# Kernel tuning notes

Measured on AMD Instinct MI355X. Metric: run time of the kernel, lower is better.

The kernel has to match this reference:

```python
import jax, jax.numpy as jnp
import numpy as np

N = 40000   # nodes
E = 640000  # edges (avg degree 16)
D = 128     # in_dim
G = 64      # graphs in batch
C = 100     # n_classes
L = 3       # hidden_layers + 1 AGNN layers
EPS = 1e-12 # F.normalize eps


def setup_inputs() -> dict:
    key = jax.random.key(0)
    ks = jax.random.split(key, 6)
    h = jax.random.normal(ks[0], (N, D), jnp.float32)
    src = jax.random.randint(ks[1], (E,), 0, N, jnp.int32)
    dst = jax.random.randint(ks[2], (E,), 0, N, jnp.int32)
    graph_ids = jnp.sort(jax.random.randint(ks[3], (N,), 0, G, jnp.int32))
    betas = jnp.ones((L,), jnp.float32)  # init_beta=1.0, one learnable beta per AGNNConv
    W_cls = jax.random.normal(ks[4], (D, C), jnp.float32) / np.sqrt(D)
    b_cls = jnp.zeros((C,), jnp.float32)
    return dict(h=h, src=src, dst=dst, graph_ids=graph_ids,
                betas=betas, W_cls=W_cls, b_cls=b_cls)


def agnn_layer(h, src, dst, beta):
    # cosine-similarity attention (DGL AGNNConv)
    nh = h / (jnp.linalg.norm(h, axis=-1, keepdims=True) + EPS)  # [N, D]
    s = beta * jnp.sum(nh[src] * nh[dst], axis=-1)               # [E] edge scores
    # segment softmax over incoming edges of each dst node
    m = jax.ops.segment_max(s, dst, num_segments=N)              # [N]
    m = jnp.where(jnp.isfinite(m), m, 0.0)                       # empty segments -> 0
    a = jnp.exp(s - m[dst])                                      # [E]
    denom = jax.ops.segment_sum(a, dst, num_segments=N)          # [N]
    num = jax.ops.segment_sum(a[:, None] * h[src], dst, num_segments=N)  # [N, D]
    return num / jnp.where(denom > 0, denom, 1.0)[:, None]


def reference(h, src, dst, graph_ids, betas, W_cls, b_cls):
    # dropout is identity at inference; batch_norms are unused in the original forward
    for l in range(L):
        h = agnn_layer(h, src, dst, betas[l])
    # AvgPooling readout: per-graph mean of node features
    hg = jax.ops.segment_sum(h, graph_ids, num_segments=G)       # [G, D]
    cnt = jax.ops.segment_sum(jnp.ones((N,), h.dtype), graph_ids, num_segments=G)
    hg = hg / jnp.maximum(cnt, 1.0)[:, None]
    return hg @ W_cls + b_cls                                    # [G, C]
```

## Files before the change

### kernel.cpp

```cpp
#include <hip/hip_runtime.h>
#include <hip/hip_fp16.h>
#include <math.h>

#define N_NODES 40000
#define N_EDGES 640000
#define DIM     128
#define N_GRAPHS 64
#define N_CLS   100
#define N_LAYERS 3
#define EPSN    1e-12f


__global__ void k_zero_int(int* __restrict__ a, int n) {
    int i = blockIdx.x * blockDim.x + threadIdx.x;
    if (i < n) a[i] = 0;
}

__global__ void k_count(const int* __restrict__ dst, int* __restrict__ counts,
                        int* __restrict__ posw) {
    int e = blockIdx.x * blockDim.x + threadIdx.x;
    if (e < N_EDGES) posw[e] = atomicAdd(&counts[dst[e]], 1);
}

#define SCAN_T 1024
#define SCAN_V 40
__global__ void k_scan(const int* __restrict__ counts, int* __restrict__ offsets) {
    __shared__ int lds[SCAN_T];
    int t = threadIdx.x;
    int base = t * SCAN_V;
    int tsum = 0;
    if (base < N_NODES) {
        for (int k = 0; k < SCAN_V; ++k) tsum += counts[base + k];
    }
    lds[t] = tsum; __syncthreads();
    int x = tsum;
    for (int off = 1; off < SCAN_T; off <<= 1) {
        int y = (t >= off) ? lds[t - off] : 0;
        __syncthreads();
        x += y;
        lds[t] = x;
        __syncthreads();
    }
    int excl = x - tsum;
    if (base < N_NODES) {
        int run = excl;
        for (int k = 0; k < SCAN_V; ++k) {
            offsets[base + k] = run;
            run += counts[base + k];
        }
    }
    if (t == (N_NODES / SCAN_V)) offsets[N_NODES] = excl;
}

__global__ void k_scatter(const int* __restrict__ src, const int* __restrict__ dst,
                          const int* __restrict__ offsets, const int* __restrict__ posw,
                          int* __restrict__ csr_src) {
    int e = blockIdx.x * blockDim.x + threadIdx.x;
    if (e >= N_EDGES) return;
    csr_src[offsets[dst[e]] + posw[e]] = src[e];
}


__global__ void k_norm(const float* __restrict__ h, float* __restrict__ inv,
                       __half2* __restrict__ hh) {
    int node = (blockIdx.x * blockDim.x + threadIdx.x) >> 6;
    int lane = threadIdx.x & 63;
    if (node >= N_NODES) return;
    const float2* r2 = (const float2*)(h + (size_t)node * DIM);
    float2 v = r2[lane];
    float ss = v.x * v.x + v.y * v.y;
    #pragma unroll
    for (int o = 32; o; o >>= 1) ss += __shfl_xor(ss, o);
    if (lane == 0) inv[node] = 1.0f / (sqrtf(ss) + EPSN);
    hh[(size_t)node * 64 + lane] = __floats2half2_rn(v.x, v.y);
}

union H8 { int4 i4; __half2 h2[4]; };

__device__ __forceinline__ void cvt8(const H8& u, float* f) {
    #pragma unroll
    for (int k = 0; k < 4; ++k) {
        float2 v = __half22float2(u.h2[k]);
        f[2 * k]     = v.x;
        f[2 * k + 1] = v.y;
    }
}

template <bool LAST>
__global__ void k_fused(const int4* __restrict__ hh_in,
                        const float* __restrict__ inv_in,
                        const int* __restrict__ csr_src,
                        const int* __restrict__ offsets,
                        const float* __restrict__ betas, int layer,
                        int4* __restrict__ hh_out,
                        float* __restrict__ inv_out,
                        const int* __restrict__ gid,
                        float* __restrict__ hgsum) {
    int node = (blockIdx.x * blockDim.x + threadIdx.x) >> 6;
    int lane = threadIdx.x & 63;
    int grp = lane >> 4;
    int t   = lane & 15;

    int off = offsets[node];
    int deg = offsets[node + 1] - off;

    size_t nrow16 = (size_t)node * 16;
    H8 selfu; selfu.i4 = hh_in[nrow16 + t];
    float hd[8]; cvt8(selfu, hd);
    float bi = betas[layer] * inv_in[node];

    float dsum = 0.f;
    float ac[8];
    #pragma unroll
    for (int k = 0; k < 8; ++k) ac[k] = 0.f;

    if (deg > 0) {
        int last = deg - 1;
        int jb = 0;
        for (; jb + 8 <= deg; jb += 8) {
            int s0 = csr_src[off + jb + grp];
            int s1 = csr_src[off + jb + 4 + grp];
            H8 u0, u1;
            u0.i4 = hh_in[(size_t)s0 * 16 + t];
            u1.i4 = hh_in[(size_t)s1 * 16 + t];
            float iv0 = inv_in[s0], iv1 = inv_in[s1];
            float f0[8], f1[8];
            cvt8(u0, f0); cvt8(u1, f1);
            float p0 = 0.f, p1 = 0.f;
            #pragma unroll
            for (int k = 0; k < 8; ++k) { p0 += f0[k] * hd[k]; p1 += f1[k] * hd[k]; }
            #pragma unroll
            for (int o = 8; o; o >>= 1) {
                p0 += __shfl_xor(p0, o);
                p1 += __shfl_xor(p1, o);
            }
            float w0 = __expf(bi * iv0 * p0);
            float w1 = __expf(bi * iv1 * p1);
            dsum += w0 + w1;
            #pragma unroll
            for (int k = 0; k < 8; ++k) ac[k] += w0 * f0[k] + w1 * f1[k];
        }
        for (; jb < deg; jb += 4) {
            int j = jb + grp;
            bool valid = j <= last;
            int idx = valid ? j : last;
            int s = csr_src[off + idx];
            H8 u; u.i4 = hh_in[(size_t)s * 16 + t];
            float iv = inv_in[s];
            float f[8]; cvt8(u, f);
            float p = 0.f;
            #pragma unroll
            for (int k = 0; k < 8; ++k) p += f[k] * hd[k];
            #pragma unroll
            for (int o = 8; o; o >>= 1) p += __shfl_xor(p, o);
            float w = valid ? __expf(bi * iv * p) : 0.f;
            dsum += w;
            #pragma unroll
            for (int k = 0; k < 8; ++k) ac[k] += w * f[k];
        }

        #pragma unroll
        for (int o = 16; o < 64; o <<= 1) {
            dsum += __shfl_xor(dsum, o);
            #pragma unroll
            for (int k = 0; k < 8; ++k) ac[k] += __shfl_xor(ac[k], o);
        }
        float invd = 1.0f / dsum;
        #pragma unroll
        for (int k = 0; k < 8; ++k) ac[k] *= invd;
    }

    if (LAST) {
        __shared__ float spool[DIM];
        __shared__ int sg[4];
        int tid = threadIdx.x;
        int g = gid[node];
        if (lane == 0) sg[tid >> 6] = g;
        if (tid < DIM) spool[tid] = 0.f;
        __syncthreads();
        bool uni = (sg[0] == sg[1]) && (sg[1] == sg[2]) && (sg[2] == sg[3]);
        if (uni) {
            if (grp == 0) {
                #pragma unroll
                for (int k = 0; k < 8; ++k) atomicAdd(&spool[8 * t + k], ac[k]);
            }
            __syncthreads();
            if (tid < DIM) atomicAdd(&hgsum[(size_t)sg[0] * DIM + tid], spool[tid]);
        } else {
            if (grp == 0) {
                #pragma unroll
                for (int k = 0; k < 8; ++k)
                    atomicAdd(&hgsum[(size_t)g * DIM + 8 * t + k], ac[k]);
            }
        }
    } else {
        if (grp == 0) {
            H8 w;
            #pragma unroll
            for (int k = 0; k < 4; ++k)
                w.h2[k] = __floats2half2_rn(ac[2 * k], ac[2 * k + 1]);
            hh_out[nrow16 + t] = w.i4;
        }
        float ss = 0.f;
        #pragma unroll
        for (int k = 0; k < 8; ++k) ss += ac[k] * ac[k];
        #pragma unroll
        for (int o = 8; o; o >>= 1) ss += __shfl_xor(ss, o);
        if (lane == 0) inv_out[node] = 1.0f / (sqrtf(ss) + EPSN);
    }
}


__global__ void k_cls(const float* __restrict__ hgsum, const int* __restrict__ gid,
                      const float* __restrict__ W, const float* __restrict__ b,
                      float* __restrict__ out) {
    int g = blockIdx.x;
    int c = threadIdx.x;
    __shared__ float invc_s;
    if (c == 0) {
        int lo = 0, hi = N_NODES;
        while (lo < hi) { int mid = (lo + hi) >> 1; if (gid[mid] < g) lo = mid + 1; else hi = mid; }
        int start = lo;
        lo = 0; hi = N_NODES;
        while (lo < hi) { int mid = (lo + hi) >> 1; if (gid[mid] < g + 1) lo = mid + 1; else hi = mid; }
        invc_s = 1.0f / fmaxf((float)(lo - start), 1.0f);
    }
    __syncthreads();
    if (c >= N_CLS) return;
    float acc = 0.f;
    #pragma unroll 8
    for (int d = 0; d < DIM; ++d) acc += hgsum[g * DIM + d] * W[d * N_CLS + c];
    out[g * N_CLS + c] = b[c] + acc * invc_s;
}


extern "C" void kernel_launch(void* const* d_in, const int* in_sizes, int n_in,
                              void* d_out, int out_size, void* d_ws, size_t ws_size,
                              hipStream_t stream) {
    const float* h_in  = (const float*)d_in[0];
    const int*   src   = (const int*)  d_in[1];
    const int*   dst   = (const int*)  d_in[2];
    const int*   gid   = (const int*)  d_in[3];
    const float* betas = (const float*)d_in[4];
    const float* W     = (const float*)d_in[5];
    const float* bcls  = (const float*)d_in[6];
    float* out = (float*)d_out;

    char* p = (char*)d_ws;
    int4*  hh0     = (int4*)p;  p += (size_t)N_NODES * DIM * 2;
    int4*  hh1     = (int4*)p;  p += (size_t)N_NODES * DIM * 2;
    float* inv0    = (float*)p; p += (size_t)N_NODES * 4;
    float* inv1    = (float*)p; p += (size_t)N_NODES * 4;
    int*   counts  = (int*)p;   p += (size_t)N_NODES * 4;
    float* hgsum   = (float*)p; p += (size_t)N_GRAPHS * DIM * 4;
    int*   offsets = (int*)p;   p += (size_t)(N_NODES + 4) * 4;
    int*   posw    = (int*)p;   p += (size_t)N_EDGES * 4;
    int*   csr_src = (int*)p;   p += (size_t)N_EDGES * 4;

    const int ZERO_N = N_NODES + N_GRAPHS * DIM;

    k_zero_int<<<(ZERO_N + 255) / 256, 256, 0, stream>>>(counts, ZERO_N);
    k_count<<<(N_EDGES + 255) / 256, 256, 0, stream>>>(dst, counts, posw);
    k_scan<<<1, SCAN_T, 0, stream>>>(counts, offsets);
    k_scatter<<<(N_EDGES + 255) / 256, 256, 0, stream>>>(src, dst, offsets, posw, csr_src);

    k_norm<<<N_NODES / 4, 256, 0, stream>>>(h_in, inv0, (__half2*)hh0);
    k_fused<false><<<N_NODES / 4, 256, 0, stream>>>(hh0, inv0, csr_src, offsets, betas, 0,
                                                    hh1, inv1, nullptr, nullptr);
    k_fused<false><<<N_NODES / 4, 256, 0, stream>>>(hh1, inv1, csr_src, offsets, betas, 1,
                                                    hh0, inv0, nullptr, nullptr);
    k_fused<true><<<N_NODES / 4, 256, 0, stream>>>(hh0, inv0, csr_src, offsets, betas, 2,
                                                   nullptr, nullptr, gid, hgsum);

    k_cls<<<N_GRAPHS, DIM, 0, stream>>>(hgsum, gid, W, bcls, out);
}
```

Measured before the change: 200.6 us.

## Store normalized fp16 features, fuse count with norm, unroll gather by 16

Measured after the change: 220.8 us. +10.1%, slower.

```diff
diff --git a/kernel.cpp b/kernel.cpp
--- a/kernel.cpp
+++ b/kernel.cpp
@@ -7,19 +7,33 @@
 #define DIM     128
 #define N_GRAPHS 64
 #define N_CLS   100
-#define N_LAYERS 3
 #define EPSN    1e-12f
 
-
-__global__ void k_zero_int(int* __restrict__ a, int n) {
-    int i = blockIdx.x * blockDim.x + threadIdx.x;
-    if (i < n) a[i] = 0;
-}
-
-__global__ void k_count(const int* __restrict__ dst, int* __restrict__ counts,
-                        int* __restrict__ posw) {
-    int e = blockIdx.x * blockDim.x + threadIdx.x;
-    if (e < N_EDGES) posw[e] = atomicAdd(&counts[dst[e]], 1);
+#define EDGE_BLOCKS ((N_EDGES + 255) / 256)
+#define NODE_BLOCKS (N_NODES / 4)
+
+
+__global__ void k_count_norm(const int* __restrict__ dst, int* __restrict__ counts,
+                             int* __restrict__ posw,
+                             const float* __restrict__ h, float* __restrict__ nrm,
+                             __half2* __restrict__ nh) {
+    int b = blockIdx.x;
+    if (b < EDGE_BLOCKS) {
+        int e = b * 256 + threadIdx.x;
+        if (e < N_EDGES) posw[e] = atomicAdd(&counts[dst[e]], 1);
+    } else {
+        int node = ((b - EDGE_BLOCKS) << 2) + (threadIdx.x >> 6);
+        int lane = threadIdx.x & 63;
+        const float2* r2 = (const float2*)(h + (size_t)node * DIM);
+        float2 v = r2[lane];
+        float ss = v.x * v.x + v.y * v.y;
+        #pragma unroll
+        for (int o = 32; o; o >>= 1) ss += __shfl_xor(ss, o);
+        float norm = sqrtf(ss) + EPSN;
+        float inv = 1.0f / norm;
+        if (lane == 0) nrm[node] = norm;
+        nh[(size_t)node * 64 + lane] = __floats2half2_rn(v.x * inv, v.y * inv);
+    }
 }
 
 #define SCAN_T 1024
@@ -61,20 +75,6 @@
 }
 
 
-__global__ void k_norm(const float* __restrict__ h, float* __restrict__ inv,
-                       __half2* __restrict__ hh) {
-    int node = (blockIdx.x * blockDim.x + threadIdx.x) >> 6;
-    int lane = threadIdx.x & 63;
-    if (node >= N_NODES) return;
-    const float2* r2 = (const float2*)(h + (size_t)node * DIM);
-    float2 v = r2[lane];
-    float ss = v.x * v.x + v.y * v.y;
-    #pragma unroll
-    for (int o = 32; o; o >>= 1) ss += __shfl_xor(ss, o);
-    if (lane == 0) inv[node] = 1.0f / (sqrtf(ss) + EPSN);
-    hh[(size_t)node * 64 + lane] = __floats2half2_rn(v.x, v.y);
-}
-
 union H8 { int4 i4; __half2 h2[4]; };
 
 __device__ __forceinline__ void cvt8(const H8& u, float* f) {
@@ -87,13 +87,13 @@
 }
 
 template <bool LAST>
-__global__ void k_fused(const int4* __restrict__ hh_in,
-                        const float* __restrict__ inv_in,
+__global__ void k_fused(const int4* __restrict__ nh_in,
+                        const float* __restrict__ nrm_in,
                         const int* __restrict__ csr_src,
                         const int* __restrict__ offsets,
                         const float* __restrict__ betas, int layer,
-                        int4* __restrict__ hh_out,
-                        float* __restrict__ inv_out,
+                        int4* __restrict__ nh_out,
+                        float* __restrict__ nrm_out,
                         const int* __restrict__ gid,
                         float* __restrict__ hgsum) {
     int node = (blockIdx.x * blockDim.x + threadIdx.x) >> 6;
@@ -105,9 +105,9 @@
     int deg = offsets[node + 1] - off;
 
     size_t nrow16 = (size_t)node * 16;
-    H8 selfu; selfu.i4 = hh_in[nrow16 + t];
+    H8 selfu; selfu.i4 = nh_in[nrow16 + t];
     float hd[8]; cvt8(selfu, hd);
-    float bi = betas[layer] * inv_in[node];
+    float beta = betas[layer];
 
     float dsum = 0.f;
     float ac[8];
@@ -117,46 +117,79 @@
     if (deg > 0) {
         int last = deg - 1;
         int jb = 0;
-        for (; jb + 8 <= deg; jb += 8) {
+        for (; jb + 16 <= deg; jb += 16) {
+            int s0 = csr_src[off + jb + grp];
+            int s1 = csr_src[off + jb + 4 + grp];
+            int s2 = csr_src[off + jb + 8 + grp];
+            int s3 = csr_src[off + jb + 12 + grp];
+            H8 u0, u1, u2, u3;
+            u0.i4 = nh_in[(size_t)s0 * 16 + t];
+            u1.i4 = nh_in[(size_t)s1 * 16 + t];
+            u2.i4 = nh_in[(size_t)s2 * 16 + t];
+            u3.i4 = nh_in[(size_t)s3 * 16 + t];
+            float n0 = nrm_in[s0], n1 = nrm_in[s1], n2 = nrm_in[s2], n3 = nrm_in[s3];
+            float f0[8], f1[8], f2[8], f3[8];
+            cvt8(u0, f0); cvt8(u1, f1); cvt8(u2, f2); cvt8(u3, f3);
+            float p0 = 0.f, p1 = 0.f, p2 = 0.f, p3 = 0.f;
+            #pragma unroll
+            for (int q = 0; q < 8; ++q) {
+                p0 += f0[q] * hd[q]; p1 += f1[q] * hd[q];
+                p2 += f2[q] * hd[q]; p3 += f3[q] * hd[q];
+            }
+            #pragma unroll
+            for (int o = 8; o; o >>= 1) {
+                p0 += __shfl_xor(p0, o); p1 += __shfl_xor(p1, o);
+                p2 += __shfl_xor(p2, o); p3 += __shfl_xor(p3, o);
+            }
+            float w0 = __expf(beta * p0), w1 = __expf(beta * p1);
+            float w2 = __expf(beta * p2), w3 = __expf(beta * p3);
+            dsum += (w0 + w1) + (w2 + w3);
+            float r0 = w0 * n0, r1 = w1 * n1, r2 = w2 * n2, r3 = w3 * n3;
+            #pragma unroll
+            for (int q = 0; q < 8; ++q)
+                ac[q] += (r0 * f0[q] + r1 * f1[q]) + (r2 * f2[q] + r3 * f3[q]);
+        }
+        if (jb + 8 <= deg) {
             int s0 = csr_src[off + jb + grp];
             int s1 = csr_src[off + jb + 4 + grp];
             H8 u0, u1;
-            u0.i4 = hh_in[(size_t)s0 * 16 + t];
-            u1.i4 = hh_in[(size_t)s1 * 16 + t];
-            float iv0 = inv_in[s0], iv1 = inv_in[s1];
+            u0.i4 = nh_in[(size_t)s0 * 16 + t];
+            u1.i4 = nh_in[(size_t)s1 * 16 + t];
+            float n0 = nrm_in[s0], n1 = nrm_in[s1];
             float f0[8], f1[8];
             cvt8(u0, f0); cvt8(u1, f1);
             float p0 = 0.f, p1 = 0.f;
             #pragma unroll
-            for (int k = 0; k < 8; ++k) { p0 += f0[k] * hd[k]; p1 += f1[k] * hd[k]; }
+            for (int q = 0; q < 8; ++q) { p0 += f0[q] * hd[q]; p1 += f1[q] * hd[q]; }
             #pragma unroll
             for (int o = 8; o; o >>= 1) {
-                p0 += __shfl_xor(p0, o);
-                p1 += __shfl_xor(p1, o);
-            }
-            float w0 = __expf(bi * iv0 * p0);
-            float w1 = __expf(bi * iv1 * p1);
+                p0 += __shfl_xor(p0, o); p1 += __shfl_xor(p1, o);
+            }
+            float w0 = __expf(beta * p0), w1 = __expf(beta * p1);
             dsum += w0 + w1;
-            #pragma unroll
-            for (int k = 0; k < 8; ++k) ac[k] += w0 * f0[k] + w1 * f1[k];
+            float r0 = w0 * n0, r1 = w1 * n1;
+            #pragma unroll
+            for (int q = 0; q < 8; ++q) ac[q] += r0 * f0[q] + r1 * f1[q];
+            jb += 8;
         }
         for (; jb < deg; jb += 4) {
-            int j = jb + grp;
-            bool valid = j <= last;
-            int idx = valid ? j : last;
-            int s = csr_src[off + idx];
-            H8 u; u.i4 = hh_in[(size_t)s * 16 + t];
-            float iv = inv_in[s];
+            int eidx = jb + grp;
+            bool vv = eidx <= last;
+            int ec = vv ? eidx : last;
+            int s = csr_src[off + ec];
+            H8 u; u.i4 = nh_in[(size_t)s * 16 + t];
+            float nr = nrm_in[s];
             float f[8]; cvt8(u, f);
             float p = 0.f;
             #pragma unroll
-            for (int k = 0; k < 8; ++k) p += f[k] * hd[k];
+            for (int q = 0; q < 8; ++q) p += f[q] * hd[q];
             #pragma unroll
             for (int o = 8; o; o >>= 1) p += __shfl_xor(p, o);
-            float w = valid ? __expf(bi * iv * p) : 0.f;
+            float w = vv ? __expf(beta * p) : 0.f;
             dsum += w;
-            #pragma unroll
-            for (int k = 0; k < 8; ++k) ac[k] += w * f[k];
+            float r = w * nr;
+            #pragma unroll
+            for (int q = 0; q < 8; ++q) ac[q] += r * f[q];
         }
 
         #pragma unroll
@@ -194,19 +227,21 @@
             }
         }
     } else {
+        float ss = 0.f;
+        #pragma unroll
+        for (int k = 0; k < 8; ++k) ss += ac[k] * ac[k];
+        #pragma unroll
+        for (int o = 8; o; o >>= 1) ss += __shfl_xor(ss, o);
+        float norm = sqrtf(ss) + EPSN;
+        float inv2 = 1.0f / norm;
         if (grp == 0) {
             H8 w;
             #pragma unroll
             for (int k = 0; k < 4; ++k)
-                w.h2[k] = __floats2half2_rn(ac[2 * k], ac[2 * k + 1]);
-            hh_out[nrow16 + t] = w.i4;
-        }
-        float ss = 0.f;
-        #pragma unroll
-        for (int k = 0; k < 8; ++k) ss += ac[k] * ac[k];
-        #pragma unroll
-        for (int o = 8; o; o >>= 1) ss += __shfl_xor(ss, o);
-        if (lane == 0) inv_out[node] = 1.0f / (sqrtf(ss) + EPSN);
+                w.h2[k] = __floats2half2_rn(ac[2 * k] * inv2, ac[2 * k + 1] * inv2);
+            nh_out[nrow16 + t] = w.i4;
+        }
+        if (lane == 0) nrm_out[node] = norm;
     }
 }
 
@@ -247,29 +282,29 @@
     float* out = (float*)d_out;
 
     char* p = (char*)d_ws;
-    int4*  hh0     = (int4*)p;  p += (size_t)N_NODES * DIM * 2;
-    int4*  hh1     = (int4*)p;  p += (size_t)N_NODES * DIM * 2;
-    float* inv0    = (float*)p; p += (size_t)N_NODES * 4;
-    float* inv1    = (float*)p; p += (size_t)N_NODES * 4;
+    int4*  nh0     = (int4*)p;  p += (size_t)N_NODES * DIM * 2;
+    int4*  nh1     = (int4*)p;  p += (size_t)N_NODES * DIM * 2;
+    float* nrm0    = (float*)p; p += (size_t)N_NODES * 4;
+    float* nrm1    = (float*)p; p += (size_t)N_NODES * 4;
     int*   counts  = (int*)p;   p += (size_t)N_NODES * 4;
     float* hgsum   = (float*)p; p += (size_t)N_GRAPHS * DIM * 4;
     int*   offsets = (int*)p;   p += (size_t)(N_NODES + 4) * 4;
     int*   posw    = (int*)p;   p += (size_t)N_EDGES * 4;
     int*   csr_src = (int*)p;   p += (size_t)N_EDGES * 4;
 
-    const int ZERO_N = N_NODES + N_GRAPHS * DIM;
-
-    k_zero_int<<<(ZERO_N + 255) / 256, 256, 0, stream>>>(counts, ZERO_N);
-    k_count<<<(N_EDGES + 255) / 256, 256, 0, stream>>>(dst, counts, posw);
+    const size_t ZERO_BYTES = (size_t)(N_NODES + N_GRAPHS * DIM) * 4;
+
+    hipMemsetAsync(counts, 0, ZERO_BYTES, stream);
+    k_count_norm<<<EDGE_BLOCKS + NODE_BLOCKS, 256, 0, stream>>>(
+        dst, counts, posw, h_in, nrm0, (__half2*)nh0);
     k_scan<<<1, SCAN_T, 0, stream>>>(counts, offsets);
     k_scatter<<<(N_EDGES + 255) / 256, 256, 0, stream>>>(src, dst, offsets, posw, csr_src);
 
-    k_norm<<<N_NODES / 4, 256, 0, stream>>>(h_in, inv0, (__half2*)hh0);
-    k_fused<false><<<N_NODES / 4, 256, 0, stream>>>(hh0, inv0, csr_src, offsets, betas, 0,
-                                                    hh1, inv1, nullptr, nullptr);
-    k_fused<false><<<N_NODES / 4, 256, 0, stream>>>(hh1, inv1, csr_src, offsets, betas, 1,
-                                                    hh0, inv0, nullptr, nullptr);
-    k_fused<true><<<N_NODES / 4, 256, 0, stream>>>(hh0, inv0, csr_src, offsets, betas, 2,
+    k_fused<false><<<N_NODES / 4, 256, 0, stream>>>(nh0, nrm0, csr_src, offsets, betas, 0,
+                                                    nh1, nrm1, nullptr, nullptr);
+    k_fused<false><<<N_NODES / 4, 256, 0, stream>>>(nh1, nrm1, csr_src, offsets, betas, 1,
+                                                    nh0, nrm0, nullptr, nullptr);
+    k_fused<true><<<N_NODES / 4, 256, 0, stream>>>(nh0, nrm0, csr_src, offsets, betas, 2,
                                                    nullptr, nullptr, gid, hgsum);
 
     k_cls<<<N_GRAPHS, DIM, 0, stream>>>(hgsum, gid, W, bcls, out);
```
